# Optimization experiments

Measured on AMD Instinct MI355X. Metric: run time of the kernel, lower is better.

Reference implementation:

```python
import jax, jax.numpy as jnp
import numpy as np

T_LATENCY = 2  # refractory latency (timesteps), from init_kwargs
FS_SCALE = 10.0  # FastSigmoid surrogate scale


@jax.custom_vjp
def fast_sigmoid_spike(u):
    return (u > 0).astype(u.dtype)

def _fs_fwd(u):
    return fast_sigmoid_spike(u), u

def _fs_bwd(u, g):
    return (g / (FS_SCALE * jnp.abs(u) + 1.0) ** 2,)

fast_sigmoid_spike.defvjp(_fs_fwd, _fs_bwd)


def setup_inputs() -> dict:
    key = jax.random.key(0)
    k1, k2, k3, k4 = jax.random.split(key, 4)
    B, N, T = 64, 1024, 512
    x = jax.random.normal(k1, (B, N, T), dtype=jnp.float32)
    beta = jax.random.uniform(k2, (N,), jnp.float32, 0.3, 0.95)   # leak
    p = jax.random.uniform(k3, (N,), jnp.float32, 0.5, 0.95)      # adaptation decay
    b = jax.random.uniform(k4, (N,), jnp.float32, 0.5, 1.5)       # adaptation strength
    return {"x": x, "beta": beta, "p": p, "b": b}


def reference(x, beta, p, b):
    # clamped effective params (matches torch @property accessors)
    beta_c = jnp.clip(beta, 0.001, 0.999)
    p_c = jnp.clip(jnp.abs(p), 0.0, 0.999)
    b_c = jnp.clip(jnp.abs(b), 0.001, 1.0)

    B, N, T = x.shape
    xt = jnp.moveaxis(x, 2, 0)  # [T, B, N]

    def step(carry, x_t):
        mem, spikes, refac, a, v_th = carry
        # spike-triggered refractory reset, then mask input during refractory window
        refac = jnp.where(spikes > 0, 0.0, refac)
        ic = jnp.where(refac < T_LATENCY, 0.0, x_t)
        refac = refac + 1.0
        # leaky integration
        new_mem = mem * beta_c + ic
        s = fast_sigmoid_spike(new_mem - v_th)
        # reset-by-subtraction-to-zero with detached spikes (detach_spike_grad=True)
        mem = new_mem * (1.0 - jax.lax.stop_gradient(s))
        # adaptive threshold
        a = p_c * a + s
        v_th = 1.0 + b_c * a
        return (mem, s, refac, a, v_th), s

    z = jnp.zeros((B, N), x.dtype)
    init = (z, z, jnp.full((B, N), float(T_LATENCY), x.dtype), z,
            jnp.ones((B, N), x.dtype))
    _, spikes_seq = jax.lax.scan(step, init, xt)  # [T, B, N]
    return jnp.moveaxis(spikes_seq, 0, 2)  # [B, N, T]
```

## Files before the change

kernel.cpp:

```cpp
#include <hip/hip_runtime.h>

#pragma clang fp contract(off)

#define ROWS    64
#define T_LEN   512
#define CHUNK   64
#define NCHUNK  (T_LEN / CHUNK)
#define STRIDE  (CHUNK + 1)
#define NV      16
#define NPARAM  1024

#define BARRIER() asm volatile("s_waitcnt lgkmcnt(0)\n\ts_barrier" ::: "memory")

__global__ __launch_bounds__(192) void snn_fwd(
    const float* __restrict__ x,
    const float* __restrict__ beta,
    const float* __restrict__ p,
    const float* __restrict__ bparam,
    float* __restrict__ out)
{
    __shared__ float inbuf[2][ROWS * STRIDE];
    __shared__ float outbuf[ROWS * STRIDE];

    const int tid     = threadIdx.x;
    const int wid     = tid >> 6;
    const int lane    = tid & 63;
    const int rowBase = blockIdx.x * ROWS;

    const float4* __restrict__ xv = (const float4*)x;
    float4* __restrict__ ov       = (float4*)out;

    const int t16 = lane & 15;
    const int r4  = lane >> 4;
    const int gq  = (rowBase + r4) * (T_LEN / 4) + t16;
    const int lf  = r4 * STRIDE + t16 * 4;

    float mem = 0.0f, refac = 2.0f, a = 0.0f, vth = 1.0f, ps = 0.0f;
    float beta_c = 0.f, p_c = 0.f, b_c = 0.f;
    const int cb = lane * STRIDE;

    if (wid == 0) {
        const int n = (rowBase + lane) & (NPARAM - 1);
        beta_c = fminf(fmaxf(beta[n], 0.001f), 0.999f);
        p_c    = fminf(fabsf(p[n]), 0.999f);
        b_c    = fminf(fmaxf(fabsf(bparam[n]), 0.001f), 1.0f);
    }

    auto step = [&](float xt) -> float {
        refac = (ps > 0.0f) ? 0.0f : refac;
        const float ic = (refac < 2.0f) ? 0.0f : xt;
        refac += 1.0f;
        const float nm   = __fadd_rn(__fmul_rn(mem, beta_c), ic);
        const float diff = __fsub_rn(nm, vth);
        const float s    = (diff > 0.0f) ? 1.0f : 0.0f;
        mem = (diff > 0.0f) ? 0.0f : nm;
        a   = __fadd_rn(__fmul_rn(p_c, a), s);
        vth = __fadd_rn(1.0f, __fmul_rn(b_c, a));
        ps  = s;
        return s;
    };

    float4 ld[NV];

    auto loadChunk = [&](int k) {
        const int base = gq + k * NV;
        #pragma unroll
        for (int it = 0; it < NV; ++it)
            ld[it] = xv[base + it * 4 * (T_LEN / 4)];
    };
    auto stage = [&](int buf) {
        #pragma unroll
        for (int it = 0; it < NV; ++it) {
            const int o = lf + it * 4 * STRIDE;
            inbuf[buf][o + 0] = ld[it].x;
            inbuf[buf][o + 1] = ld[it].y;
            inbuf[buf][o + 2] = ld[it].z;
            inbuf[buf][o + 3] = ld[it].w;
        }
    };
    auto drain = [&](int k) {
        const int base = gq + k * NV;
        #pragma unroll
        for (int it = 0; it < NV; ++it) {
            const int o = lf + it * 4 * STRIDE;
            float4 sv;
            sv.x = outbuf[o + 0];
            sv.y = outbuf[o + 1];
            sv.z = outbuf[o + 2];
            sv.w = outbuf[o + 3];
            ov[base + it * 4 * (T_LEN / 4)] = sv;
        }
    };

    if (wid == 1) {
        loadChunk(0);
        stage(0);
        loadChunk(1);
    }
    BARRIER();

    #pragma unroll 1
    for (int k = 0; k < NCHUNK; ++k) {
        const int cur = k & 1;
        float sv[CHUNK];
        if (wid == 0) {
            #pragma unroll
            for (int t = 0; t < CHUNK; ++t)
                sv[t] = step(inbuf[cur][cb + t]);
        } else if (wid == 1) {
            if (k + 1 < NCHUNK) stage(cur ^ 1);
            if (k + 2 < NCHUNK) loadChunk(k + 2);
        } else {
            if (k > 0) drain(k - 1);
        }
        BARRIER();
        if (wid == 0) {
            #pragma unroll
            for (int t = 0; t < CHUNK; ++t)
                outbuf[cb + t] = sv[t];
        }
        BARRIER();
    }
    if (wid == 2) drain(NCHUNK - 1);
}

extern "C" void kernel_launch(void* const* d_in, const int* in_sizes, int n_in,
                              void* d_out, int out_size, void* d_ws, size_t ws_size,
                              hipStream_t stream) {
    const float* x    = (const float*)d_in[0];
    const float* beta = (const float*)d_in[1];
    const float* p    = (const float*)d_in[2];
    const float* b    = (const float*)d_in[3];
    float* out        = (float*)d_out;

    const int BN = 64 * 1024;
    snn_fwd<<<dim3(BN / ROWS), dim3(192), 0, stream>>>(x, beta, p, b, out);
}
```

Measured before the change: 241.4 us.

## Pack spikes as bytes, add second loader wave, drop per-chunk second barrier

```diff
diff --git a/kernel.cpp b/kernel.cpp
--- a/kernel.cpp
+++ b/kernel.cpp
@@ -6,21 +6,22 @@
 #define T_LEN   512
 #define CHUNK   64
 #define NCHUNK  (T_LEN / CHUNK)
-#define STRIDE  (CHUNK + 1)
+#define STRIDE  68
+#define WSTRIDE 20
 #define NV      16
 #define NPARAM  1024
 
 #define BARRIER() asm volatile("s_waitcnt lgkmcnt(0)\n\ts_barrier" ::: "memory")
 
-__global__ __launch_bounds__(192) void snn_fwd(
+__global__ __launch_bounds__(256) void snn_fwd(
     const float* __restrict__ x,
     const float* __restrict__ beta,
     const float* __restrict__ p,
     const float* __restrict__ bparam,
     float* __restrict__ out)
 {
-    __shared__ float inbuf[2][ROWS * STRIDE];
-    __shared__ float outbuf[ROWS * STRIDE];
+    __shared__ __align__(16) float        inbuf[2][ROWS * STRIDE];
+    __shared__ __align__(16) unsigned int outw [2][ROWS * WSTRIDE];
 
     const int tid     = threadIdx.x;
     const int wid     = tid >> 6;
@@ -37,7 +38,6 @@
 
     float mem = 0.0f, refac = 2.0f, a = 0.0f, vth = 1.0f, ps = 0.0f;
     float beta_c = 0.f, p_c = 0.f, b_c = 0.f;
-    const int cb = lane * STRIDE;
 
     if (wid == 0) {
         const int n = (rowBase + lane) & (NPARAM - 1);
@@ -70,58 +70,68 @@
     };
     auto stage = [&](int buf) {
         #pragma unroll
-        for (int it = 0; it < NV; ++it) {
-            const int o = lf + it * 4 * STRIDE;
-            inbuf[buf][o + 0] = ld[it].x;
-            inbuf[buf][o + 1] = ld[it].y;
-            inbuf[buf][o + 2] = ld[it].z;
-            inbuf[buf][o + 3] = ld[it].w;
-        }
+        for (int it = 0; it < NV; ++it)
+            *(float4*)&inbuf[buf][lf + it * 4 * STRIDE] = ld[it];
     };
     auto drain = [&](int k) {
+        const int buf  = k & 1;
         const int base = gq + k * NV;
         #pragma unroll
         for (int it = 0; it < NV; ++it) {
-            const int o = lf + it * 4 * STRIDE;
-            float4 sv;
-            sv.x = outbuf[o + 0];
-            sv.y = outbuf[o + 1];
-            sv.z = outbuf[o + 2];
-            sv.w = outbuf[o + 3];
-            ov[base + it * 4 * (T_LEN / 4)] = sv;
+            const unsigned int u = outw[buf][(r4 + 4 * it) * WSTRIDE + t16];
+            float4 f;
+            f.x = (u & 0x000000ffu) ? 1.0f : 0.0f;
+            f.y = (u & 0x0000ff00u) ? 1.0f : 0.0f;
+            f.z = (u & 0x00ff0000u) ? 1.0f : 0.0f;
+            f.w = (u & 0xff000000u) ? 1.0f : 0.0f;
+            ov[base + it * 4 * (T_LEN / 4)] = f;
         }
     };
 
     if (wid == 1) {
         loadChunk(0);
         stage(0);
+        loadChunk(2);
+    } else if (wid == 2) {
         loadChunk(1);
     }
     BARRIER();
 
+    const int cb4 = lane * STRIDE;
+    const int wb  = lane * WSTRIDE;
+
     #pragma unroll 1
     for (int k = 0; k < NCHUNK; ++k) {
         const int cur = k & 1;
-        float sv[CHUNK];
         if (wid == 0) {
+            float4 xq[16];
             #pragma unroll
-            for (int t = 0; t < CHUNK; ++t)
-                sv[t] = step(inbuf[cur][cb + t]);
-        } else if (wid == 1) {
-            if (k + 1 < NCHUNK) stage(cur ^ 1);
-            if (k + 2 < NCHUNK) loadChunk(k + 2);
+            for (int c = 0; c < 16; ++c)
+                xq[c] = *(const float4*)&inbuf[cur][cb4 + 4 * c];
+            unsigned int wpk[16];
+            #pragma unroll
+            for (int c = 0; c < 16; ++c) {
+                const unsigned sx = (unsigned)step(xq[c].x);
+                const unsigned sy = (unsigned)step(xq[c].y);
+                const unsigned sz = (unsigned)step(xq[c].z);
+                const unsigned sw = (unsigned)step(xq[c].w);
+                wpk[c] = sx | (sy << 8) | (sz << 16) | (sw << 24);
+            }
+            #pragma unroll
+            for (int q = 0; q < 4; ++q)
+                *(uint4*)&outw[cur][wb + 4 * q] =
+                    make_uint4(wpk[4*q], wpk[4*q+1], wpk[4*q+2], wpk[4*q+3]);
+        } else if (wid == 1 || wid == 2) {
+            if (((k + 1) & 1) == (wid - 1)) {
+                if (k + 1 < NCHUNK) stage((k + 1) & 1);
+                if (k + 3 < NCHUNK) loadChunk(k + 3);
+            }
         } else {
             if (k > 0) drain(k - 1);
         }
         BARRIER();
-        if (wid == 0) {
-            #pragma unroll
-            for (int t = 0; t < CHUNK; ++t)
-                outbuf[cb + t] = sv[t];
-        }
-        BARRIER();
     }
-    if (wid == 2) drain(NCHUNK - 1);
+    if (wid == 3) drain(NCHUNK - 1);
 }
 
 extern "C" void kernel_launch(void* const* d_in, const int* in_sizes, int n_in,
@@ -134,5 +144,5 @@
     float* out        = (float*)d_out;
 
     const int BN = 64 * 1024;
-    snn_fwd<<<dim3(BN / ROWS), dim3(192), 0, stream>>>(x, beta, p, b, out);
+    snn_fwd<<<dim3(BN / ROWS), dim3(256), 0, stream>>>(x, beta, p, b, out);
 }
```

Result: slower. 259.8 us (+7.7%).
